# Kernel tuning notes

Hardware: AMD Instinct MI355X
Metric: run time of the kernel (lower is better)

The kernel has to match this reference:

```python
import jax, jax.numpy as jnp
import numpy as np

B, S, H, D, HID = 2, 2048, 16, 64, 512
INTER = 2 * HID
EPS = 1e-8
SCALE = D ** -0.5
ROPE_THETA = 10000.0


def setup_inputs() -> dict:
    key = jax.random.key(0)
    ks = jax.random.split(key, 12)
    x = jax.random.normal(ks[0], (B, S, HID), dtype=jnp.float32)
    # RoPE tables: angles[s, i] = s / theta^(2i/D), half-dim = D//2
    inv_freq = 1.0 / (ROPE_THETA ** (jnp.arange(0, D, 2, dtype=jnp.float32) / D))  # [D/2]
    ang = jnp.arange(S, dtype=jnp.float32)[:, None] * inv_freq[None, :]            # [S, D/2]
    cos_val = jnp.cos(ang)[None, None]  # [1,1,S,D/2]
    sin_val = jnp.sin(ang)[None, None]
    # additive causal mask
    i = jnp.arange(S)
    causal_mask = jnp.where(i[None, :] > i[:, None], -1e9, 0.0).astype(jnp.float32)[None, None]
    std = 0.02
    wq = jax.random.normal(ks[1], (HID, H * D), dtype=jnp.float32) * std
    wk = jax.random.normal(ks[2], (HID, H * D), dtype=jnp.float32) * std
    wv = jax.random.normal(ks[3], (HID, H * D), dtype=jnp.float32) * std
    wo = jax.random.normal(ks[4], (H * D, HID), dtype=jnp.float32) * std
    w_gate = jax.random.normal(ks[5], (HID, INTER), dtype=jnp.float32) * std
    w_up = jax.random.normal(ks[6], (HID, INTER), dtype=jnp.float32) * std
    w_down = jax.random.normal(ks[7], (INTER, HID), dtype=jnp.float32) * std
    norm1_w = jnp.ones((HID,), dtype=jnp.float32)
    norm2_w = jnp.ones((HID,), dtype=jnp.float32)
    ls_attn = jnp.full((HID,), 0.01, dtype=jnp.float32)
    ls_mlp = jnp.full((HID,), 0.01, dtype=jnp.float32)
    return {"x": x, "cos_val": cos_val, "sin_val": sin_val, "causal_mask": causal_mask,
            "wq": wq, "wk": wk, "wv": wv, "wo": wo,
            "w_gate": w_gate, "w_up": w_up, "w_down": w_down,
            "norm1_w": norm1_w, "norm2_w": norm2_w, "ls_attn": ls_attn, "ls_mlp": ls_mlp}


def _rmsnorm(x, w):
    return x * jax.lax.rsqrt(jnp.mean(x * x, axis=-1, keepdims=True) + EPS) * w


def _rope(t, cos_val, sin_val):
    # t: [B,H,S,D]; rotate-half style with concat halves
    t1, t2 = t[..., : D // 2], t[..., D // 2 :]
    return jnp.concatenate([t1 * cos_val - t2 * sin_val, t2 * cos_val + t1 * sin_val], axis=-1)


def reference(x, cos_val, sin_val, causal_mask, wq, wk, wv, wo,
              w_gate, w_up, w_down, norm1_w, norm2_w, ls_attn, ls_mlp):
    residual = x
    h = _rmsnorm(x, norm1_w)  # [B,S,HID]
    q = (h @ wq).reshape(B, S, H, D).transpose(0, 2, 1, 3)  # [B,H,S,D]
    k = (h @ wk).reshape(B, S, H, D).transpose(0, 2, 1, 3)
    v = (h @ wv).reshape(B, S, H, D).transpose(0, 2, 1, 3)
    q = _rope(q, cos_val, sin_val)
    k = _rope(k, cos_val, sin_val)
    scores = jnp.einsum("bhqd,bhkd->bhqk", q, k) * SCALE + causal_mask
    attn = jax.nn.softmax(scores, axis=-1)
    out = jnp.einsum("bhqk,bhkd->bhqd", attn, v)  # [B,H,S,D]
    out = out.transpose(0, 2, 1, 3).reshape(B, S, H * D)
    attn_out = (out @ wo) * ls_attn  # LayerScale == per-channel scale
    h = residual + attn_out
    residual2 = h
    g = _rmsnorm(h, norm2_w)
    m = jax.nn.silu(g @ w_gate) * (g @ w_up)  # SwiGLU
    m = (m @ w_down) * ls_mlp
    return residual2 + m
```

## Files before the change

kernel.cpp:

```cpp
#include <hip/hip_runtime.h>
#include <hip/hip_bf16.h>

typedef __bf16 bf16x8 __attribute__((ext_vector_type(8)));
typedef __bf16 bf16x4 __attribute__((ext_vector_type(4)));
typedef float f32x4 __attribute__((ext_vector_type(4)));

#define SEQ   2048
#define NB    2
#define NTOK  4096
#define HIDD  512
#define NHEAD 16
#define DHEAD 64
#define QKVN  3072
#define GUN   2048

#define OFF_WQKVT  0u
#define OFF_WOT    3145728u
#define OFF_WGUT   4194304u
#define OFF_WDT    6291456u
#define OFF_HB     7340032u
#define OFF_QKV    11534336u
#define OFF_ATTN   36700160u
#define OFF_H2     45088768u
#define OFF_G      53477376u
#define OFF_M      (OFF_QKV + 16777216u)

#define QSCALE 0.1803368801111731f

#if __has_builtin(__builtin_amdgcn_exp2f)
#define EXP2(x) __builtin_amdgcn_exp2f(x)
#else
#define EXP2(x) exp2f(x)
#endif

typedef unsigned int __attribute__((address_space(1))) as1_uint;
typedef unsigned int __attribute__((address_space(3))) as3_uint;
__device__ __forceinline__ void gload16(const void* g, void* l) {
    __builtin_amdgcn_global_load_lds((const as1_uint*)g, (as3_uint*)l, 16, 0, 0);
}

__global__ __launch_bounds__(256) void prep_k(
    const float* __restrict__ wq, const float* __restrict__ wk,
    const float* __restrict__ wv, const float* __restrict__ wo,
    const float* __restrict__ wg, const float* __restrict__ wu,
    const float* __restrict__ wd,
    __bf16* __restrict__ qkvT, __bf16* __restrict__ woT,
    __bf16* __restrict__ wguT, __bf16* __restrict__ wdT,
    const float* __restrict__ x, const float* __restrict__ norm1,
    __bf16* __restrict__ hb) {
    __shared__ float t[32][33];
    int bid = blockIdx.x;
    if (bid < 3584) {
        int which = bid >> 9, bx = bid & 511;
        const float* in; __bf16* out; int K, N, mode = 0, phase = 0;
        switch (which) {
            case 0: in = wq; out = qkvT;              K = 512;  N = 1024; break;
            case 1: in = wk; out = qkvT + 1024 * 512; K = 512;  N = 1024; break;
            case 2: in = wv; out = qkvT + 2048 * 512; K = 512;  N = 1024; break;
            case 3: in = wo; out = woT;               K = 1024; N = 512;  break;
            case 4: in = wg; out = wguT;              K = 512;  N = 1024; mode = 1; phase = 0; break;
            case 5: in = wu; out = wguT;              K = 512;  N = 1024; mode = 1; phase = 1; break;
            default: in = wd; out = wdT;              K = 1024; N = 512;  break;
        }
        int ntn = N >> 5;
        int n0 = (bx & (ntn - 1)) * 32;
        int k0 = (bx / ntn) * 32;
        int tx = threadIdx.x & 31, ty = threadIdx.x >> 5;
#pragma unroll
        for (int j = 0; j < 4; ++j)
            t[ty * 4 + j][tx] = in[(size_t)(k0 + ty * 4 + j) * N + n0 + tx];
        __syncthreads();
#pragma unroll
        for (int j = 0; j < 4; ++j) {
            int n = n0 + ty * 4 + j;
            int row = mode ? (((n >> 4) << 5) + phase * 16 + (n & 15)) : n;
            out[(size_t)row * K + k0 + tx] = (__bf16)t[tx][ty * 4 + j];
        }
    } else {
        int row = bid - 3584;
        int tt = threadIdx.x;
        const float* xr = x + (size_t)row * HIDD;
        float2 v = *(const float2*)&xr[tt * 2];
        float ss = v.x * v.x + v.y * v.y;
#pragma unroll
        for (int off = 32; off >= 1; off >>= 1) ss += __shfl_xor(ss, off);
        if ((tt & 63) == 0) t[0][tt >> 6] = ss;
        __syncthreads();
        float tot = t[0][0] + t[0][1] + t[0][2] + t[0][3];
        float r = rsqrtf(tot * (1.0f / HIDD) + 1e-8f);
        hb[(size_t)row * HIDD + tt * 2]     = (__bf16)(v.x * r * norm1[tt * 2]);
        hb[(size_t)row * HIDD + tt * 2 + 1] = (__bf16)(v.y * r * norm1[tt * 2 + 1]);
    }
}

__global__ __launch_bounds__(256) void rmsnorm_k(const float* __restrict__ x,
                                                 const float* __restrict__ w,
                                                 __bf16* __restrict__ out) {
    int row = blockIdx.x;
    int t = threadIdx.x;
    const float* xr = x + (size_t)row * HIDD;
    float2 v = *(const float2*)&xr[t * 2];
    float ss = v.x * v.x + v.y * v.y;
#pragma unroll
    for (int off = 32; off >= 1; off >>= 1) ss += __shfl_xor(ss, off);
    __shared__ float red[4];
    if ((t & 63) == 0) red[t >> 6] = ss;
    __syncthreads();
    float tot = red[0] + red[1] + red[2] + red[3];
    float r = rsqrtf(tot * (1.0f / HIDD) + 1e-8f);
    out[(size_t)row * HIDD + t * 2]     = (__bf16)(v.x * r * w[t * 2]);
    out[(size_t)row * HIDD + t * 2 + 1] = (__bf16)(v.y * r * w[t * 2 + 1]);
}

template <int EPI, int TM, int TN, int BK>
__global__ __launch_bounds__(256) void gemm_bt(const __bf16* __restrict__ A,
                                               const __bf16* __restrict__ Bt,
                                               int M, int N, int K,
                                               __bf16* __restrict__ Cb,
                                               float* __restrict__ Cf,
                                               const float* __restrict__ resid,
                                               const float* __restrict__ scale,
                                               const float* __restrict__ cosv,
                                               const float* __restrict__ sinv) {
    __shared__ alignas(16) __bf16 As[TM][BK];
    __shared__ alignas(16) __bf16 Bs[TN][BK];
    constexpr int MI = TM / 32, NI = TN / 32;
    constexpr int CPB = BK / 8;
    int nwg = gridDim.x * gridDim.y;
    int bid = blockIdx.y * gridDim.x + blockIdx.x;
    int swz = (bid & 7) * (nwg >> 3) + (bid >> 3);
    int bx = swz % gridDim.x, by = swz / gridDim.x;
    int m0 = by * TM, n0 = bx * TN;
    int tid = threadIdx.x;
    int lane = tid & 63, w = tid >> 6;
    int wm = (w >> 1) * (TM / 2), wn = (w & 1) * (TN / 2);
    int lr = lane & 15, lkg = lane >> 4;
    f32x4 acc[MI][NI] = {};
    int nkt = K / BK;
    for (int kt = 0; kt < nkt; ++kt) {
        __syncthreads();
#pragma unroll
        for (int i = 0; i < (TM * BK) / 2048; ++i) {
            int c = i * 256 + tid;
            int row = c / CPB, ch = c % CPB;
            gload16(&A[(size_t)(m0 + row) * K + kt * BK + ((ch ^ (row & 7)) << 3)],
                    (__bf16*)As + c * 8);
        }
#pragma unroll
        for (int i = 0; i < (TN * BK) / 2048; ++i) {
            int c = i * 256 + tid;
            int row = c / CPB, ch = c % CPB;
            gload16(&Bt[(size_t)(n0 + row) * K + kt * BK + ((ch ^ (row & 7)) << 3)],
                    (__bf16*)Bs + c * 8);
        }
        __syncthreads();
#pragma unroll
        for (int kk = 0; kk < BK / 32; ++kk) {
            bf16x8 af[MI], bfv[NI];
#pragma unroll
            for (int mi = 0; mi < MI; ++mi) {
                int row = wm + mi * 16 + lr;
                af[mi] = *(const bf16x8*)&As[row][(((kk * 4 + lkg) ^ (row & 7)) << 3)];
            }
#pragma unroll
            for (int ni = 0; ni < NI; ++ni) {
                int row = wn + ni * 16 + lr;
                bfv[ni] = *(const bf16x8*)&Bs[row][(((kk * 4 + lkg) ^ (row & 7)) << 3)];
            }
#pragma unroll
            for (int mi = 0; mi < MI; ++mi)
#pragma unroll
                for (int ni = 0; ni < NI; ++ni)
                    acc[mi][ni] = __builtin_amdgcn_mfma_f32_16x16x32_bf16(
                        af[mi], bfv[ni], acc[mi][ni], 0, 0, 0);
        }
    }
    if (EPI == 1) {
        bool do_rope = (n0 + wn) < 2048;
        float qf = (n0 + wn) < 1024 ? QSCALE : 1.0f;
#pragma unroll
        for (int mi = 0; mi < MI; ++mi)
#pragma unroll
            for (int r = 0; r < 4; ++r) {
                int row = m0 + wm + mi * 16 + (lane >> 4) * 4 + r;
                int s = row & (SEQ - 1);
#pragma unroll
                for (int ni = 0; ni < 2; ++ni) {
                    float v1 = acc[mi][ni][r], v2 = acc[mi][ni + 2][r];
                    size_t i1 = (size_t)row * N + n0 + wn + ni * 16 + lr;
                    size_t i2 = i1 + 32;
                    if (do_rope) {
                        int d = ni * 16 + lr;
                        float c = cosv[s * 32 + d], sn = sinv[s * 32 + d];
                        Cb[i1] = (__bf16)((v1 * c - v2 * sn) * qf);
                        Cb[i2] = (__bf16)((v2 * c + v1 * sn) * qf);
                    } else {
                        Cb[i1] = (__bf16)v1;
                        Cb[i2] = (__bf16)v2;
                    }
                }
            }
    } else if (EPI == 3) {
#pragma unroll
        for (int mi = 0; mi < MI; ++mi)
#pragma unroll
            for (int r = 0; r < 4; ++r) {
                int row = m0 + wm + mi * 16 + (lane >> 4) * 4 + r;
#pragma unroll
                for (int ni = 0; ni < 4; ni += 2) {
                    float g = acc[mi][ni][r], u = acc[mi][ni + 1][r];
                    float mv = (g / (1.0f + __expf(-g))) * u;
                    int j = (((n0 + wn + ni * 16) >> 5) << 4) + lr;
                    Cb[(size_t)row * 1024 + j] = (__bf16)mv;
                }
            }
    } else {
#pragma unroll
        for (int mi = 0; mi < MI; ++mi)
#pragma unroll
            for (int ni = 0; ni < NI; ++ni)
#pragma unroll
                for (int r = 0; r < 4; ++r) {
                    int row = m0 + wm + mi * 16 + (lane >> 4) * 4 + r;
                    int col = n0 + wn + ni * 16 + lr;
                    size_t idx = (size_t)row * N + col;
                    float vv = acc[mi][ni][r];
                    if (EPI == 0) Cb[idx] = (__bf16)vv;
                    else          Cf[idx] = resid[idx] + vv * scale[col];
                }
    }
}

__global__ __launch_bounds__(256) void kvprep_k(const __bf16* __restrict__ qkv,
                                                __bf16* __restrict__ kb,
                                                __bf16* __restrict__ vtb) {
    __shared__ __bf16 tr[64 * 132];
    int bh = blockIdx.x, st = blockIdx.y;
    int b = bh >> 4, h = bh & 15;
    size_t tok0 = (size_t)b * SEQ + st * 128;
    int tid = threadIdx.x;
#pragma unroll
    for (int i = 0; i < 4; ++i) {
        int c = i * 256 + tid;
        int kr = c >> 3, ch = c & 7;
        uint4 v = *(const uint4*)&qkv[(tok0 + kr) * QKVN + 1024 + h * 64 + ch * 8];
        *(uint4*)&kb[((size_t)bh * SEQ + st * 128 + kr) * 64 + ch * 8] = v;
    }
#pragma unroll
    for (int i = 0; i < 4; ++i) {
        int c = i * 256 + tid;
        int vr = c >> 3, ch = c & 7;
        uint4 v = *(const uint4*)&qkv[(tok0 + vr) * QKVN + 2048 + h * 64 + ch * 8];
        const __bf16* ve = (const __bf16*)&v;
#pragma unroll
        for (int j = 0; j < 8; ++j) tr[(ch * 8 + j) * 132 + vr] = ve[j];
    }
    __syncthreads();
#pragma unroll
    for (int i = 0; i < 4; ++i) {
        int c = i * 256 + tid;
        int dv = c >> 4, rest = c & 15;
        int t64 = rest >> 3, cc = rest & 7;
        int K0 = t64 * 64 + 32 * (cc >> 2) + 4 * (cc & 3);
        __bf16 outv[8];
#pragma unroll
        for (int j = 0; j < 4; ++j) outv[j] = tr[dv * 132 + K0 + j];
#pragma unroll
        for (int j = 0; j < 4; ++j) outv[4 + j] = tr[dv * 132 + K0 + 16 + j];
        *(uint4*)&vtb[((size_t)bh * 64 + dv) * SEQ + st * 128 + t64 * 64 + cc * 8] =
            *(uint4*)outv;
    }
}

__global__ __launch_bounds__(512, 4) void attn_k(const __bf16* __restrict__ qkv,
                                                 const __bf16* __restrict__ kb,
                                                 const __bf16* __restrict__ vtb,
                                                 __bf16* __restrict__ outp) {
    __shared__ alignas(16) __bf16 KS[2][2][4096];
    __shared__ alignas(16) __bf16 VS[2][2][4096];
    int bh = blockIdx.x;
    int b = bh >> 4, h = bh & 15;
    int y = blockIdx.y;
    int qbA = y, qbB = 31 - y;
    int TA = y + 1;
    int tid = threadIdx.x;
    int grp = tid >> 8;
    int tg  = tid & 255;
    int lane = tid & 63, wg = tg >> 6;
    int lq = lane & 15, g = lane >> 4;
    size_t tokb = (size_t)b * SEQ;
    int qr0A = qbA * 64 + wg * 16, qr0B = qbB * 64 + wg * 16;

    bf16x8 ones8;
#pragma unroll
    for (int e = 0; e < 8; ++e) ones8[e] = (__bf16)1.0f;

    f32x4 oa[4] = {};
    f32x4 ol = {};

#define STAGE_K(kbn, kdst)                                                                         \
    {                                                                                              \
        _Pragma("unroll")                                                                          \
        for (int i = 0; i < 2; ++i) {                                                              \
            int c = i * 256 + tg;                                                                  \
            int kr = c >> 3, ch = c & 7;                                                           \
            gload16(&kb[((size_t)bh * SEQ + (kbn) * 64 + kr) * 64 + ((ch ^ (kr & 7)) << 3)],       \
                    (kdst) + c * 8);                                                               \
        }                                                                                          \
    }

#define STAGE_V(kbn, vdst)                                                                         \
    {                                                                                              \
        _Pragma("unroll")                                                                          \
        for (int i = 0; i < 2; ++i) {                                                              \
            int c = i * 256 + tg;                                                                  \
            int vr = c >> 3, ch = c & 7;                                                           \
            gload16(&vtb[((size_t)bh * 64 + vr) * SEQ + (kbn) * 64 + ((ch ^ (vr & 7)) << 3)],      \
                    (vdst) + c * 8);                                                               \
        }                                                                                          \
    }

#define QK_S(sc, aq, ksrc)                                                                         \
    {                                                                                              \
        __builtin_amdgcn_s_setprio(1);                                                             \
        _Pragma("unroll")                                                                          \
        for (int jt = 0; jt < 4; ++jt)                                                             \
            _Pragma("unroll")                                                                      \
            for (int ks = 0; ks < 2; ++ks) {                                                       \
                bf16x8 bk = *(const bf16x8*)&(ksrc)[(jt * 16 + lq) * 64 + (((ks * 4 + g) ^ (lq & 7)) << 3)]; \
                sc[jt] = __builtin_amdgcn_mfma_f32_16x16x32_bf16(bk, aq[ks], sc[jt], 0, 0, 0);     \
            }                                                                                      \
        __builtin_amdgcn_s_setprio(0);                                                             \
    }

#define MASK_S(sc, qr0_t, kb64)                                                                    \
    {                                                                                              \
        int qabs = (qr0_t) + lq;                                                                   \
        _Pragma("unroll")                                                                          \
        for (int jt = 0; jt < 4; ++jt)                                                             \
            _Pragma("unroll")                                                                      \
            for (int r = 0; r < 4; ++r) {                                                          \
                int key = (kb64) * 64 + jt * 16 + g * 4 + r;                                       \
                if (key > qabs) sc[jt][r] = -1e9f;                                                 \
            }                                                                                      \
    }

#define EXP_S(sc)                                                                                  \
    _Pragma("unroll")                                                                              \
    for (int jt = 0; jt < 4; ++jt)                                                                 \
        _Pragma("unroll")                                                                          \
        for (int r = 0; r < 4; ++r) sc[jt][r] = EXP2(sc[jt][r]);

#define PV_S(sc, vsrc)                                                                             \
    {                                                                                              \
        __builtin_amdgcn_s_setprio(1);                                                             \
        _Pragma("unroll")                                                                          \
        for (int ks2 = 0; ks2 < 2; ++ks2) {                                                        \
            bf16x8 pfv;                                                                            \
            _Pragma("unroll")                                                                      \
            for (int e = 0; e < 4; ++e) {                                                          \
                pfv[e]     = (__bf16)sc[2 * ks2][e];                                               \
                pfv[e + 4] = (__bf16)sc[2 * ks2 + 1][e];                                           \
            }                                                                                      \
            ol = __builtin_amdgcn_mfma_f32_16x16x32_bf16(ones8, pfv, ol, 0, 0, 0);                 \
            _Pragma("unroll")                                                                      \
            for (int dt = 0; dt < 4; ++dt) {                                                       \
                bf16x8 av = *(const bf16x8*)&(vsrc)[(dt * 16 + lq) * 64 + (((ks2 * 4 + g) ^ (lq & 7)) << 3)]; \
                oa[dt] = __builtin_amdgcn_mfma_f32_16x16x32_bf16(av, pfv, oa[dt], 0, 0, 0);        \
            }                                                                                      \
        }                                                                                          \
        __builtin_amdgcn_s_setprio(0);                                                             \
    }

    if (grp == 0) {
        bf16x8 aqB[2];
#pragma unroll
        for (int ks = 0; ks < 2; ++ks)
            aqB[ks] = *(const bf16x8*)&qkv[(tokb + qr0B + lq) * QKVN + h * 64 + ks * 32 + g * 8];
        STAGE_K(0, KS[0][0]);
        STAGE_V(0, VS[0][0]);
        __syncthreads();
        for (int it = 0; it < 17; ++it) {
            int buf = it & 1;
            bool pf = it < 16;
            if (pf) {
                STAGE_K(it + 1, KS[0][buf ^ 1]);
                STAGE_V(it + 1, VS[0][buf ^ 1]);
            }
            f32x4 sc[4] = {};
            QK_S(sc, aqB, KS[0][buf]);
            if (it == qbB) MASK_S(sc, qr0B, it);
            EXP_S(sc);
            PV_S(sc, VS[0][buf]);
            __syncthreads();
        }
    } else {
        {
            bf16x8 aqA[2];
#pragma unroll
            for (int ks = 0; ks < 2; ++ks)
                aqA[ks] = *(const bf16x8*)&qkv[(tokb + qr0A + lq) * QKVN + h * 64 + ks * 32 + g * 8];
            __syncthreads();
            for (int it = 0; it < TA; ++it) {
                int buf = it & 1;
                if (it == TA - 1) {
                    STAGE_K(17, KS[1][0]);
                    STAGE_V(17, VS[1][0]);
                }
                f32x4 sc[4] = {};
                QK_S(sc, aqA, KS[0][buf]);
                if (it == qbA) MASK_S(sc, qr0A, it);
                EXP_S(sc);
                PV_S(sc, VS[0][buf]);
                __syncthreads();
            }
        }
        {
            float inv = 1.0f / ol[0];
#pragma unroll
            for (int dt = 0; dt < 4; ++dt) {
                bf16x4 ov;
#pragma unroll
                for (int r = 0; r < 4; ++r) ov[r] = (__bf16)(oa[dt][r] * inv);
                *(bf16x4*)&outp[(tokb + qr0A + lq) * 1024 + h * 64 + dt * 16 + g * 4] = ov;
                oa[dt] = (f32x4){0.f, 0.f, 0.f, 0.f};
            }
            ol = (f32x4){0.f, 0.f, 0.f, 0.f};
        }
        {
            bf16x8 aqB[2];
#pragma unroll
            for (int ks = 0; ks < 2; ++ks)
                aqB[ks] = *(const bf16x8*)&qkv[(tokb + qr0B + lq) * QKVN + h * 64 + ks * 32 + g * 8];
            int cnt = 16 - TA;
            for (int j = 0; j < cnt; ++j) {
                int buf = j & 1;
                if (j + 1 < cnt) {
                    STAGE_K(17 + j + 1, KS[1][buf ^ 1]);
                    STAGE_V(17 + j + 1, VS[1][buf ^ 1]);
                }
                f32x4 sc[4] = {};
                int kb64 = 17 + j;
                QK_S(sc, aqB, KS[1][buf]);
                if (kb64 == qbB) MASK_S(sc, qr0B, kb64);
                EXP_S(sc);
                PV_S(sc, VS[1][buf]);
                __syncthreads();
            }
        }
        __syncthreads();
    }

    float* mrg_oa = (float*)KS[1];
    float* mrg_ol = (float*)VS[1];
    if (grp == 1) {
#pragma unroll
        for (int dt = 0; dt < 4; ++dt)
#pragma unroll
            for (int r = 0; r < 4; ++r) mrg_oa[tg * 16 + dt * 4 + r] = oa[dt][r];
        mrg_ol[tg] = ol[0];
    }
    __syncthreads();
    if (grp == 0) {
        float l = ol[0] + mrg_ol[tg];
        float inv = 1.0f / l;
#pragma unroll
        for (int dt = 0; dt < 4; ++dt) {
            bf16x4 ov;
#pragma unroll
            for (int r = 0; r < 4; ++r)
                ov[r] = (__bf16)((oa[dt][r] + mrg_oa[tg * 16 + dt * 4 + r]) * inv);
            *(bf16x4*)&outp[(tokb + qr0B + lq) * 1024 + h * 64 + dt * 16 + g * 4] = ov;
        }
    }
#undef STAGE_K
#undef STAGE_V
#undef QK_S
#undef MASK_S
#undef EXP_S
#undef PV_S
}

extern "C" void kernel_launch(void* const* d_in, const int* in_sizes, int n_in,
                              void* d_out, int out_size, void* d_ws, size_t ws_size,
                              hipStream_t stream) {
    const float* x       = (const float*)d_in[0];
    const float* cosv    = (const float*)d_in[1];
    const float* sinv    = (const float*)d_in[2];
    const float* wq      = (const float*)d_in[4];
    const float* wk      = (const float*)d_in[5];
    const float* wv      = (const float*)d_in[6];
    const float* wo      = (const float*)d_in[7];
    const float* wgate   = (const float*)d_in[8];
    const float* wup     = (const float*)d_in[9];
    const float* wdown   = (const float*)d_in[10];
    const float* norm1   = (const float*)d_in[11];
    const float* norm2   = (const float*)d_in[12];
    const float* ls_attn = (const float*)d_in[13];
    const float* ls_mlp  = (const float*)d_in[14];

    char* ws = (char*)d_ws;
    __bf16* wqkvT = (__bf16*)(ws + OFF_WQKVT);
    __bf16* woT   = (__bf16*)(ws + OFF_WOT);
    __bf16* wguT  = (__bf16*)(ws + OFF_WGUT);
    __bf16* wdT   = (__bf16*)(ws + OFF_WDT);
    __bf16* hb    = (__bf16*)(ws + OFF_HB);
    __bf16* qkvb  = (__bf16*)(ws + OFF_QKV);
    __bf16* attnb = (__bf16*)(ws + OFF_ATTN);
    float*  h2    = (float*)(ws + OFF_H2);
    __bf16* kbuf  = (__bf16*)(ws + OFF_H2);
    __bf16* vtbuf = (__bf16*)(ws + OFF_M);
    __bf16* gb    = (__bf16*)(ws + OFF_G);
    __bf16* mb    = (__bf16*)(ws + OFF_M);
    float*  outf  = (float*)d_out;

    prep_k<<<7680, 256, 0, stream>>>(
        wq, wk, wv, wo, wgate, wup, wdown, wqkvT, woT, wguT, wdT, x, norm1, hb);
    gemm_bt<1, 128, 128, 64><<<dim3(QKVN / 128, NTOK / 128), 256, 0, stream>>>(
        hb, wqkvT, NTOK, QKVN, 512, qkvb, nullptr, nullptr, nullptr, cosv, sinv);
    kvprep_k<<<dim3(NB * NHEAD, SEQ / 128), 256, 0, stream>>>(qkvb, kbuf, vtbuf);
    attn_k<<<dim3(NB * NHEAD, 16), 512, 0, stream>>>(qkvb, kbuf, vtbuf, attnb);
    gemm_bt<2, 64, 64, 128><<<dim3(HIDD / 64, NTOK / 64), 256, 0, stream>>>(
        attnb, woT, NTOK, HIDD, 1024, nullptr, h2, x, ls_attn, nullptr, nullptr);
    rmsnorm_k<<<NTOK, 256, 0, stream>>>(h2, norm2, gb);
    gemm_bt<3, 128, 128, 64><<<dim3(GUN / 128, NTOK / 128), 256, 0, stream>>>(
        gb, wguT, NTOK, GUN, 512, mb, nullptr, nullptr, nullptr, nullptr, nullptr);
    gemm_bt<2, 64, 64, 128><<<dim3(HIDD / 64, NTOK / 64), 256, 0, stream>>>(
        mb, wdT, NTOK, HIDD, 1024, nullptr, outf, h2, ls_mlp, nullptr, nullptr);
}
```

Before: 111.9 us.

## Write Q/K/V directly in head-major layout and store residual h2 as bf16

```diff
diff --git a/kernel.cpp b/kernel.cpp
--- a/kernel.cpp
+++ b/kernel.cpp
@@ -19,11 +19,13 @@
 #define OFF_WGUT   4194304u
 #define OFF_WDT    6291456u
 #define OFF_HB     7340032u
-#define OFF_QKV    11534336u
+#define OFF_QB     11534336u
+#define OFF_KB     (OFF_QB + 8388608u)
+#define OFF_VB     (OFF_QB + 16777216u)
 #define OFF_ATTN   36700160u
 #define OFF_H2     45088768u
 #define OFF_G      53477376u
-#define OFF_M      (OFF_QKV + 16777216u)
+#define OFF_M      OFF_VB
 
 #define QSCALE 0.1803368801111731f
 
@@ -93,14 +95,14 @@
     }
 }
 
-__global__ __launch_bounds__(256) void rmsnorm_k(const float* __restrict__ x,
-                                                 const float* __restrict__ w,
-                                                 __bf16* __restrict__ out) {
+__global__ __launch_bounds__(256) void rmsnorm_bk(const __bf16* __restrict__ x,
+                                                  const float* __restrict__ w,
+                                                  __bf16* __restrict__ out) {
     int row = blockIdx.x;
     int t = threadIdx.x;
-    const float* xr = x + (size_t)row * HIDD;
-    float2 v = *(const float2*)&xr[t * 2];
-    float ss = v.x * v.x + v.y * v.y;
+    const __bf16* xr = x + (size_t)row * HIDD;
+    float v0 = (float)xr[t * 2], v1 = (float)xr[t * 2 + 1];
+    float ss = v0 * v0 + v1 * v1;
 #pragma unroll
     for (int off = 32; off >= 1; off >>= 1) ss += __shfl_xor(ss, off);
     __shared__ float red[4];
@@ -108,8 +110,8 @@
     __syncthreads();
     float tot = red[0] + red[1] + red[2] + red[3];
     float r = rsqrtf(tot * (1.0f / HIDD) + 1e-8f);
-    out[(size_t)row * HIDD + t * 2]     = (__bf16)(v.x * r * w[t * 2]);
-    out[(size_t)row * HIDD + t * 2 + 1] = (__bf16)(v.y * r * w[t * 2 + 1]);
+    out[(size_t)row * HIDD + t * 2]     = (__bf16)(v0 * r * w[t * 2]);
+    out[(size_t)row * HIDD + t * 2 + 1] = (__bf16)(v1 * r * w[t * 2 + 1]);
 }
 
 template <int EPI, int TM, int TN, int BK>
@@ -121,7 +123,9 @@
                                                const float* __restrict__ resid,
                                                const float* __restrict__ scale,
                                                const float* __restrict__ cosv,
-                                               const float* __restrict__ sinv) {
+                                               const float* __restrict__ sinv,
+                                               __bf16* __restrict__ kbp,
+                                               __bf16* __restrict__ vbp) {
     __shared__ alignas(16) __bf16 As[TM][BK];
     __shared__ alignas(16) __bf16 Bs[TN][BK];
     constexpr int MI = TM / 32, NI = TN / 32;
@@ -176,28 +180,38 @@
         }
     }
     if (EPI == 1) {
-        bool do_rope = (n0 + wn) < 2048;
-        float qf = (n0 + wn) < 1024 ? QSCALE : 1.0f;
+        int col0 = n0 + wn;
+        int hh = (col0 >> 6) & 15;
 #pragma unroll
         for (int mi = 0; mi < MI; ++mi)
 #pragma unroll
             for (int r = 0; r < 4; ++r) {
-                int row = m0 + wm + mi * 16 + (lane >> 4) * 4 + r;
+                int row = m0 + wm + mi * 16 + lkg * 4 + r;
                 int s = row & (SEQ - 1);
-#pragma unroll
-                for (int ni = 0; ni < 2; ++ni) {
-                    float v1 = acc[mi][ni][r], v2 = acc[mi][ni + 2][r];
-                    size_t i1 = (size_t)row * N + n0 + wn + ni * 16 + lr;
-                    size_t i2 = i1 + 32;
-                    if (do_rope) {
+                size_t hdr = ((size_t)((row >> 11) * 16 + hh) * SEQ + s) * 64;
+                if (col0 < 1024) {
+#pragma unroll
+                    for (int ni = 0; ni < 2; ++ni) {
+                        float v1 = acc[mi][ni][r], v2 = acc[mi][ni + 2][r];
                         int d = ni * 16 + lr;
                         float c = cosv[s * 32 + d], sn = sinv[s * 32 + d];
-                        Cb[i1] = (__bf16)((v1 * c - v2 * sn) * qf);
-                        Cb[i2] = (__bf16)((v2 * c + v1 * sn) * qf);
-                    } else {
-                        Cb[i1] = (__bf16)v1;
-                        Cb[i2] = (__bf16)v2;
+                        size_t i1 = (size_t)row * 1024 + col0 + d;
+                        Cb[i1]      = (__bf16)((v1 * c - v2 * sn) * QSCALE);
+                        Cb[i1 + 32] = (__bf16)((v2 * c + v1 * sn) * QSCALE);
                     }
+                } else if (col0 < 2048) {
+#pragma unroll
+                    for (int ni = 0; ni < 2; ++ni) {
+                        float v1 = acc[mi][ni][r], v2 = acc[mi][ni + 2][r];
+                        int d = ni * 16 + lr;
+                        float c = cosv[s * 32 + d], sn = sinv[s * 32 + d];
+                        kbp[hdr + d]      = (__bf16)(v1 * c - v2 * sn);
+                        kbp[hdr + d + 32] = (__bf16)(v2 * c + v1 * sn);
+                    }
+                } else {
+#pragma unroll
+                    for (int ni = 0; ni < 4; ++ni)
+                        vbp[hdr + ni * 16 + lr] = (__bf16)acc[mi][ni][r];
                 }
             }
     } else if (EPI == 3) {
@@ -205,7 +219,7 @@
         for (int mi = 0; mi < MI; ++mi)
 #pragma unroll
             for (int r = 0; r < 4; ++r) {
-                int row = m0 + wm + mi * 16 + (lane >> 4) * 4 + r;
+                int row = m0 + wm + mi * 16 + lkg * 4 + r;
 #pragma unroll
                 for (int ni = 0; ni < 4; ni += 2) {
                     float g = acc[mi][ni][r], u = acc[mi][ni + 1][r];
@@ -214,43 +228,45 @@
                     Cb[(size_t)row * 1024 + j] = (__bf16)mv;
                 }
             }
-    } else {
+    } else if (EPI == 4) {
 #pragma unroll
         for (int mi = 0; mi < MI; ++mi)
 #pragma unroll
             for (int ni = 0; ni < NI; ++ni)
 #pragma unroll
                 for (int r = 0; r < 4; ++r) {
-                    int row = m0 + wm + mi * 16 + (lane >> 4) * 4 + r;
+                    int row = m0 + wm + mi * 16 + lkg * 4 + r;
                     int col = n0 + wn + ni * 16 + lr;
                     size_t idx = (size_t)row * N + col;
-                    float vv = acc[mi][ni][r];
-                    if (EPI == 0) Cb[idx] = (__bf16)vv;
-                    else          Cf[idx] = resid[idx] + vv * scale[col];
+                    Cb[idx] = (__bf16)(resid[idx] + acc[mi][ni][r] * scale[col]);
                 }
-    }
-}
-
-__global__ __launch_bounds__(256) void kvprep_k(const __bf16* __restrict__ qkv,
-                                                __bf16* __restrict__ kb,
+    } else if (EPI == 5) {
+        const __bf16* rb = (const __bf16*)Cb;
+#pragma unroll
+        for (int mi = 0; mi < MI; ++mi)
+#pragma unroll
+            for (int ni = 0; ni < NI; ++ni)
+#pragma unroll
+                for (int r = 0; r < 4; ++r) {
+                    int row = m0 + wm + mi * 16 + lkg * 4 + r;
+                    int col = n0 + wn + ni * 16 + lr;
+                    size_t idx = (size_t)row * N + col;
+                    Cf[idx] = (float)rb[idx] + acc[mi][ni][r] * scale[col];
+                }
+    }
+}
+
+__global__ __launch_bounds__(256) void kvprep_k(const __bf16* __restrict__ vb,
                                                 __bf16* __restrict__ vtb) {
     __shared__ __bf16 tr[64 * 132];
     int bh = blockIdx.x, st = blockIdx.y;
-    int b = bh >> 4, h = bh & 15;
-    size_t tok0 = (size_t)b * SEQ + st * 128;
     int tid = threadIdx.x;
-#pragma unroll
-    for (int i = 0; i < 4; ++i) {
-        int c = i * 256 + tid;
-        int kr = c >> 3, ch = c & 7;
-        uint4 v = *(const uint4*)&qkv[(tok0 + kr) * QKVN + 1024 + h * 64 + ch * 8];
-        *(uint4*)&kb[((size_t)bh * SEQ + st * 128 + kr) * 64 + ch * 8] = v;
-    }
+    size_t base = ((size_t)bh * SEQ + st * 128) * 64;
 #pragma unroll
     for (int i = 0; i < 4; ++i) {
         int c = i * 256 + tid;
         int vr = c >> 3, ch = c & 7;
-        uint4 v = *(const uint4*)&qkv[(tok0 + vr) * QKVN + 2048 + h * 64 + ch * 8];
+        uint4 v = *(const uint4*)&vb[base + (size_t)vr * 64 + ch * 8];
         const __bf16* ve = (const __bf16*)&v;
 #pragma unroll
         for (int j = 0; j < 8; ++j) tr[(ch * 8 + j) * 132 + vr] = ve[j];
@@ -272,7 +288,7 @@
     }
 }
 
-__global__ __launch_bounds__(512, 4) void attn_k(const __bf16* __restrict__ qkv,
+__global__ __launch_bounds__(512, 4) void attn_k(const __bf16* __restrict__ qb,
                                                  const __bf16* __restrict__ kb,
                                                  const __bf16* __restrict__ vtb,
                                                  __bf16* __restrict__ outp) {
@@ -376,7 +392,7 @@
         bf16x8 aqB[2];
 #pragma unroll
         for (int ks = 0; ks < 2; ++ks)
-            aqB[ks] = *(const bf16x8*)&qkv[(tokb + qr0B + lq) * QKVN + h * 64 + ks * 32 + g * 8];
+            aqB[ks] = *(const bf16x8*)&qb[(tokb + qr0B + lq) * 1024 + h * 64 + ks * 32 + g * 8];
         STAGE_K(0, KS[0][0]);
         STAGE_V(0, VS[0][0]);
         __syncthreads();
@@ -399,7 +415,7 @@
             bf16x8 aqA[2];
 #pragma unroll
             for (int ks = 0; ks < 2; ++ks)
-                aqA[ks] = *(const bf16x8*)&qkv[(tokb + qr0A + lq) * QKVN + h * 64 + ks * 32 + g * 8];
+                aqA[ks] = *(const bf16x8*)&qb[(tokb + qr0A + lq) * 1024 + h * 64 + ks * 32 + g * 8];
             __syncthreads();
             for (int it = 0; it < TA; ++it) {
                 int buf = it & 1;
@@ -431,7 +447,7 @@
             bf16x8 aqB[2];
 #pragma unroll
             for (int ks = 0; ks < 2; ++ks)
-                aqB[ks] = *(const bf16x8*)&qkv[(tokb + qr0B + lq) * QKVN + h * 64 + ks * 32 + g * 8];
+                aqB[ks] = *(const bf16x8*)&qb[(tokb + qr0B + lq) * 1024 + h * 64 + ks * 32 + g * 8];
             int cnt = 16 - TA;
             for (int j = 0; j < cnt; ++j) {
                 int buf = j & 1;
@@ -505,11 +521,12 @@
     __bf16* wguT  = (__bf16*)(ws + OFF_WGUT);
     __bf16* wdT   = (__bf16*)(ws + OFF_WDT);
     __bf16* hb    = (__bf16*)(ws + OFF_HB);
-    __bf16* qkvb  = (__bf16*)(ws + OFF_QKV);
+    __bf16* qbuf  = (__bf16*)(ws + OFF_QB);
+    __bf16* kbuf  = (__bf16*)(ws + OFF_KB);
+    __bf16* vbuf  = (__bf16*)(ws + OFF_VB);
+    __bf16* vtbuf = (__bf16*)(ws + OFF_H2);
     __bf16* attnb = (__bf16*)(ws + OFF_ATTN);
-    float*  h2    = (float*)(ws + OFF_H2);
-    __bf16* kbuf  = (__bf16*)(ws + OFF_H2);
-    __bf16* vtbuf = (__bf16*)(ws + OFF_M);
+    __bf16* h2b   = (__bf16*)(ws + OFF_H2);
     __bf16* gb    = (__bf16*)(ws + OFF_G);
     __bf16* mb    = (__bf16*)(ws + OFF_M);
     float*  outf  = (float*)d_out;
@@ -517,14 +534,14 @@
     prep_k<<<7680, 256, 0, stream>>>(
         wq, wk, wv, wo, wgate, wup, wdown, wqkvT, woT, wguT, wdT, x, norm1, hb);
     gemm_bt<1, 128, 128, 64><<<dim3(QKVN / 128, NTOK / 128), 256, 0, stream>>>(
-        hb, wqkvT, NTOK, QKVN, 512, qkvb, nullptr, nullptr, nullptr, cosv, sinv);
-    kvprep_k<<<dim3(NB * NHEAD, SEQ / 128), 256, 0, stream>>>(qkvb, kbuf, vtbuf);
-    attn_k<<<dim3(NB * NHEAD, 16), 512, 0, stream>>>(qkvb, kbuf, vtbuf, attnb);
-    gemm_bt<2, 64, 64, 128><<<dim3(HIDD / 64, NTOK / 64), 256, 0, stream>>>(
-        attnb, woT, NTOK, HIDD, 1024, nullptr, h2, x, ls_attn, nullptr, nullptr);
-    rmsnorm_k<<<NTOK, 256, 0, stream>>>(h2, norm2, gb);
+        hb, wqkvT, NTOK, QKVN, 512, qbuf, nullptr, nullptr, nullptr, cosv, sinv, kbuf, vbuf);
+    kvprep_k<<<dim3(NB * NHEAD, SEQ / 128), 256, 0, stream>>>(vbuf, vtbuf);
+    attn_k<<<dim3(NB * NHEAD, 16), 512, 0, stream>>>(qbuf, kbuf, vtbuf, attnb);
+    gemm_bt<4, 64, 64, 128><<<dim3(HIDD / 64, NTOK / 64), 256, 0, stream>>>(
+        attnb, woT, NTOK, HIDD, 1024, h2b, nullptr, x, ls_attn, nullptr, nullptr, nullptr, nullptr);
+    rmsnorm_bk<<<NTOK, 256, 0, stream>>>(h2b, norm2, gb);
     gemm_bt<3, 128, 128, 64><<<dim3(GUN / 128, NTOK / 128), 256, 0, stream>>>(
-        gb, wguT, NTOK, GUN, 512, mb, nullptr, nullptr, nullptr, nullptr, nullptr);
-    gemm_bt<2, 64, 64, 128><<<dim3(HIDD / 64, NTOK / 64), 256, 0, stream>>>(
-        mb, wdT, NTOK, HIDD, 1024, nullptr, outf, h2, ls_mlp, nullptr, nullptr);
-}
+        gb, wguT, NTOK, GUN, 512, mb, nullptr, nullptr, nullptr, nullptr, nullptr, nullptr, nullptr);
+    gemm_bt<5, 64, 64, 128><<<dim3(HIDD / 64, NTOK / 64), 256, 0, stream>>>(
+        mb, wdT, NTOK, HIDD, 1024, h2b, outf, nullptr, ls_mlp, nullptr, nullptr, nullptr, nullptr);
+}
```

After: 105.6 us. -5.6%, faster.
